# Performance work log

Measured on AMD Instinct MI355X. Metric: run time of the kernel, lower is better.

## Reference

```python
import jax, jax.numpy as jnp
import numpy as np

N, E, O, C, D_IN, OUT, L, B = 10000, 80000, 10, 64, 16, 16, 2, 16
DEG, WIDEN, BD = 3, 4, 64
EPS = 1e-6


def fibonacci_sphere(n):
    # deterministic near-uniform grid of n unit vectors on S^2 (stands in for GridGenerator's repulsion grid)
    i = jnp.arange(n, dtype=jnp.float32) + 0.5
    phi = jnp.arccos(1.0 - 2.0 * i / n)
    theta = jnp.pi * (1.0 + 5.0 ** 0.5) * i
    return jnp.stack([jnp.cos(theta) * jnp.sin(phi), jnp.sin(theta) * jnp.sin(phi), jnp.cos(phi)], axis=-1)


def poly_features(x, degree):
    # PolynomialFeatures: concat x, x(x)x, x(x)x(x)x, ... flattened outer products
    feats = [x]
    cur = x
    for _ in range(degree):
        cur = (cur[..., :, None] * x[..., None, :]).reshape(x.shape[:-1] + (-1,))
        feats.append(cur)
    return jnp.concatenate(feats, axis=-1)


def layer_norm(x, scale, bias):
    mu = jnp.mean(x, axis=-1, keepdims=True)
    var = jnp.mean((x - mu) ** 2, axis=-1, keepdims=True)
    return (x - mu) * jax.lax.rsqrt(var + EPS) * scale + bias


def setup_inputs():
    key = jax.random.key(0)
    ks = jax.random.split(key, 16)
    def w(k, shape):
        return jax.random.normal(k, shape, dtype=jnp.float32) / np.sqrt(shape[-2])
    P_SP = 2 + 4 + 8 + 16  # poly features of 2-dim spatial invariants, degree 3
    P_OR = 4               # poly features of 1-dim orientation invariant, degree 3
    return {
        "x": jax.random.normal(ks[0], (N, D_IN), jnp.float32),
        "pos": jax.random.normal(ks[1], (N, 3), jnp.float32),
        "basis_w1": w(ks[2], (P_SP, C)), "basis_b1": jnp.zeros((C,), jnp.float32),
        "basis_w2": w(ks[3], (C, BD)), "basis_b2": jnp.zeros((BD,), jnp.float32),
        "fbasis_w1": w(ks[4], (P_OR, C)), "fbasis_b1": jnp.zeros((C,), jnp.float32),
        "fbasis_w2": w(ks[5], (C, BD)), "fbasis_b2": jnp.zeros((BD,), jnp.float32),
        "embed_w": w(ks[6], (D_IN, C)),
        "conv_kw": w(ks[7], (L, BD, C)),
        "conv_fw": w(ks[8], (L, BD, C)),
        "conv_b": jnp.zeros((L, C), jnp.float32),
        "norm_s": jnp.ones((L, C), jnp.float32),
        "norm_b": jnp.zeros((L, C), jnp.float32),
        "lin1_w": w(ks[9], (L, C, WIDEN * C)), "lin1_b": jnp.zeros((L, WIDEN * C), jnp.float32),
        "lin2_w": w(ks[10], (L, WIDEN * C, C)), "lin2_b": jnp.zeros((L, C), jnp.float32),
        "ro_w": w(ks[11], (L, C, OUT)), "ro_b": jnp.zeros((L, OUT), jnp.float32),
        "edge_index": jax.random.randint(ks[12], (2, E), 0, N, jnp.int32),
        "batch": jnp.sort(jax.random.randint(ks[13], (N,), 0, B, jnp.int32)),
    }


def reference(x, pos, basis_w1, basis_b1, basis_w2, basis_b2, fbasis_w1, fbasis_b1, fbasis_w2, fbasis_b2, embed_w, conv_kw, conv_fw, conv_b, norm_s, norm_b, lin1_w, lin1_b, lin2_w, lin2_b, ro_w, ro_b, edge_index, batch):
    ori = fibonacci_sphere(O)                                             # [O,3]
    send, recv = edge_index[0], edge_index[1]
    rel = (pos[send] - pos[recv])[:, None, :]                              # [E,1,3]
    inv1 = jnp.sum(rel * ori[None], axis=-1, keepdims=True)                # [E,O,1]
    inv2 = jnp.linalg.norm(rel - inv1 * ori[None], axis=-1, keepdims=True) # [E,O,1]
    inv3 = jnp.sum(ori[None, :, :] * ori[:, None, :], axis=-1, keepdims=True)  # [O,O,1]
    sp = jnp.concatenate([inv1, inv2], axis=-1)                            # [E,O,2]
    kb = jax.nn.gelu(poly_features(sp, DEG) @ basis_w1 + basis_b1)
    kb = jax.nn.gelu(kb @ basis_w2 + basis_b2)                             # [E,O,BD]
    fkb = jax.nn.gelu(poly_features(inv3, DEG) @ fbasis_w1 + fbasis_b1)
    fkb = jax.nn.gelu(fkb @ fbasis_w2 + fbasis_b2)                         # [O,O,BD]
    h = jnp.broadcast_to((x @ embed_w)[:, None, :], (N, O, C))             # [N,O,C]
    readout = jnp.zeros((N, O, OUT), h.dtype)
    for l in range(L):
        # depthwise spatial conv: gather-send, modulate by kernel, scatter-add to receivers
        msg = h[send] * (kb @ conv_kw[l])                                  # [E,O,C]
        h1 = jax.ops.segment_sum(msg, recv, num_segments=N)                # [N,O,C]
        # depthwise fiber (orientation) conv
        fk = fkb @ conv_fw[l]                                              # [O,O,C]
        h2 = jnp.einsum('noc,poc->npc', h1, fk) / O + conv_b[l]
        # ConvNeXt MLP + residual
        y = layer_norm(h2, norm_s[l], norm_b[l])
        y = jax.nn.gelu(y @ lin1_w[l] + lin1_b[l]) @ lin2_w[l] + lin2_b[l]
        h = h + y
        readout = readout + (h @ ro_w[l] + ro_b[l])
    readout = readout / L
    out_scalar = jnp.mean(readout, axis=-2)                                # [N,OUT]
    pooled = jnp.zeros((B, OUT), out_scalar.dtype).at[batch].add(out_scalar)
    return pooled
```

## Files before the change

### kernel.cpp

```cpp
#include <hip/hip_runtime.h>
#include <math.h>

#define N_   10000
#define E_   80000
#define O_   10
#define B_   16
#define OUT_ 16
#define NROW_ (N_*O_)
#define NITEM_ (E_*O_)

typedef __attribute__((ext_vector_type(8))) short bf16x8;
typedef __attribute__((ext_vector_type(4))) short bf16x4;
typedef __attribute__((ext_vector_type(4))) float f32x4;

#define MFMA16(a,b,c) __builtin_amdgcn_mfma_f32_16x16x32_bf16(a,b,c,0,0,0)

__device__ __forceinline__ float gelu_f(float x) {
    float u = fmaf(0.044715f, x * x, 1.0f);
    float e = __builtin_amdgcn_exp2f(2.3022083f * x * u);
    float r = __builtin_amdgcn_rcpf(e + 1.0f);
    return fmaf(-x, r, x);
}

__device__ __forceinline__ unsigned short f2bf(float f) {
    union { float f; unsigned int u; } v; v.f = f;
    unsigned int r = v.u + 0x7FFFu + ((v.u >> 16) & 1u);
    return (unsigned short)(r >> 16);
}
__device__ __forceinline__ float bf2f(unsigned short u) {
    union { unsigned int u; float f; } v; v.u = ((unsigned int)u) << 16;
    return v.f;
}
__device__ __forceinline__ unsigned int cvtpk(float lo, float hi) {
    unsigned int r;
    asm("v_cvt_pk_bf16_f32 %0, %1, %2" : "=v"(r) : "v"(lo), "v"(hi));
    return r;
}
__device__ __forceinline__ bf16x4 pack4(float a, float b, float c, float d) {
    union { unsigned int u[2]; bf16x4 v; } z;
    z.u[0] = cvtpk(a, b);
    z.u[1] = cvtpk(c, d);
    return z.v;
}

__device__ __forceinline__ void fib_vec(int idx, float& vx, float& vy, float& vz) {
    float i = (float)idx + 0.5f;
    float phi = acosf(1.0f - 2.0f * i / (float)O_);
    float theta = 3.14159265358979323846f * (1.0f + 2.2360679774997896964f) * i;
    float sp = sinf(phi);
    vx = cosf(theta) * sp; vy = sinf(theta) * sp; vz = cosf(phi);
}

__global__ __launch_bounds__(256) void k_pack(
    const float* __restrict__ bw1, const float* __restrict__ bw2,
    const float* __restrict__ ckw, const float* __restrict__ l1w,
    const float* __restrict__ l2w, const float* __restrict__ row_w,
    float* __restrict__ orig,
    unsigned short* __restrict__ wW1P, unsigned short* __restrict__ wW2P,
    unsigned short* __restrict__ wCKP, unsigned short* __restrict__ wL1P,
    unsigned short* __restrict__ wL2P, unsigned short* __restrict__ wROP)
{
    const int g = blockIdx.x * 256 + threadIdx.x;
    if (g < 2048) {
        int idx = g;
        int t = idx >> 9, rem = idx & 511;
        int ln = rem >> 3, j = rem & 7;
        int row = t*16 + (ln & 15);
        int k = (ln >> 4)*8 + j;
        float s = 0.0f;
        if (k < 14) {
            const int moff[14] = {0,1,2,3,5,6,7,10,13,14,15,19,25,29};
            const int mcnt[14] = {1,1,1,2,1,1,3,3,1,1,4,6,4,1};
            const int mlist[30] = {0,1,2,3,4,5,6,7,8,10,9,11,12,13,14,
                                   15,16,18,22,17,19,20,23,24,26,21,25,27,28,29};
            for (int q = 0; q < mcnt[k]; ++q) s += bw1[mlist[moff[k]+q]*64 + row];
        }
        wW1P[idx] = f2bf(s);
    } else if (g < 6144) {
        int idx = g - 2048;
        int t = idx >> 9, rem = idx & 511;
        int mt = t >> 1, ks = t & 1;
        int ln = rem >> 3, j = rem & 7;
        int row = mt*16 + (ln & 15);
        int k = ks*32 + (ln >> 4)*8 + j;
        wW2P[idx] = f2bf(bw2[k*64 + row]);
    } else if (g < 14336) {
        int idx = g - 6144;
        int l = idx >> 12, r2 = idx & 4095;
        int t = r2 >> 9, rem = r2 & 511;
        int mt = t >> 1, ks = t & 1;
        int ln = rem >> 3, j = rem & 7;
        int row = mt*16 + (ln & 15);
        int k = ks*32 + (ln >> 4)*8 + j;
        wCKP[idx] = f2bf(ckw[l*4096 + k*64 + row]);
    } else if (g < 47104) {
        int idx = g - 14336;
        int l = idx >> 14, r2 = idx & 16383;
        int t = r2 >> 9, rem = r2 & 511;
        int mt = t >> 1, ks = t & 1;
        int ln = rem >> 3, j = rem & 7;
        int row = mt*16 + (ln & 15);
        int k = ks*32 + (ln >> 4)*8 + j;
        wL1P[idx] = f2bf(l1w[l*16384 + k*256 + row]);
    } else if (g < 79872) {
        int idx = g - 47104;
        int l = idx >> 14, r2 = idx & 16383;
        int t = r2 >> 9, rem = r2 & 511;
        int mt2 = t >> 3, ksg = t & 7;
        int ln = rem >> 3, j = rem & 7;
        int row = mt2*16 + (ln & 15);
        int k = ksg*32 + (ln >> 4)*8 + j;
        wL2P[idx] = f2bf(l2w[l*16384 + k*64 + row]);
    } else if (g < 81920) {
        int idx = g - 79872;
        int l = idx >> 10, r2 = idx & 1023;
        int ks = r2 >> 9, rem = r2 & 511;
        int ln = rem >> 3, j = rem & 7;
        int row = ln & 15;
        int k = ks*32 + (ln >> 4)*8 + j;
        wROP[idx] = f2bf(row_w[l*1024 + k*16 + row]);
    } else if (g < 81920 + O_) {
        int o = g - 81920;
        float vx, vy, vz;
        fib_vec(o, vx, vy, vz);
        orig[o*3+0] = vx; orig[o*3+1] = vy; orig[o*3+2] = vz;
    }
}

__global__ __launch_bounds__(256) void k_fibpre(
    const float* __restrict__ fw1, const float* __restrict__ fb1,
    const float* __restrict__ fw2, const float* __restrict__ fb2,
    const float* __restrict__ cfw, float* __restrict__ fkg)
{
    __shared__ float sRow[4][64];
    const int wv = threadIdx.x >> 6, lane = threadIdx.x & 63;
    const int pr = blockIdx.x * 4 + wv;
    if (pr >= 100) return;
    const int i = pr / O_, j = pr % O_;
    float ix, iy, iz, jx, jy, jz;
    fib_vec(i, ix, iy, iz);
    fib_vec(j, jx, jy, jz);
    float a = ix*jx + iy*jy + iz*jz;
    float a2 = a*a, a3 = a2*a, a4 = a3*a;
    float v = fb1[lane];
    v = fmaf(a,  fw1[0*64+lane], v);
    v = fmaf(a2, fw1[1*64+lane], v);
    v = fmaf(a3, fw1[2*64+lane], v);
    v = fmaf(a4, fw1[3*64+lane], v);
    sRow[wv][lane] = gelu_f(v);
    float acc = fb2[lane];
    for (int b = 0; b < 64; ++b) acc = fmaf(sRow[wv][b], fw2[b*64+lane], acc);
    sRow[wv][lane] = gelu_f(acc);
    for (int l = 0; l < 2; ++l) {
        float s = 0.0f;
        for (int b = 0; b < 64; ++b) s = fmaf(sRow[wv][b], cfw[l*4096 + b*64 + lane], s);
        fkg[l*6400 + pr*64 + lane] = s;
    }
}

__global__ __launch_bounds__(256) void k_embed(
    const float* __restrict__ x, const float* __restrict__ ew,
    float* __restrict__ hg, unsigned short* __restrict__ hbf0)
{
    int t = blockIdx.x * 256 + threadIdx.x;
    if (t >= N_ * 64) return;
    int n = t >> 6, c = t & 63;
    float v = 0.0f;
#pragma unroll
    for (int k = 0; k < 16; ++k) v = fmaf(x[n*16+k], ew[k*64+c], v);
    int base = n * 640 + c;
#pragma unroll
    for (int o = 0; o < O_; ++o) hg[base + o*64] = v;
    hbf0[t] = f2bf(v);
}

__global__ __launch_bounds__(256) void k_hist(const int* __restrict__ ei, int* __restrict__ counts)
{
    int e = blockIdx.x * 256 + threadIdx.x;
    if (e < E_) atomicAdd(&counts[ei[E_ + e]], 1);
}

__global__ __launch_bounds__(1024) void k_scan(
    const int* __restrict__ counts, int* __restrict__ offs, int* __restrict__ cursor)
{
    __shared__ int part[1024];
    int t = threadIdx.x;
    const int CH = 10;
    int base_i = t * CH;
    int s = 0;
#pragma unroll
    for (int i = 0; i < CH; ++i) { int idx = base_i + i; if (idx < N_) s += counts[idx]; }
    part[t] = s;
    __syncthreads();
    for (int off = 1; off < 1024; off <<= 1) {
        int v = (t >= off) ? part[t - off] : 0;
        __syncthreads();
        part[t] += v;
        __syncthreads();
    }
    int run = (t > 0) ? part[t - 1] : 0;
#pragma unroll
    for (int i = 0; i < CH; ++i) {
        int idx = base_i + i;
        if (idx < N_) { offs[idx] = run; cursor[idx] = run; run += counts[idx]; }
    }
    if (t == 1023) offs[N_] = run;
}

__global__ __launch_bounds__(256) void k_scatter(
    const int* __restrict__ ei, const float* __restrict__ pos,
    int* __restrict__ cursor, int* __restrict__ csend, int* __restrict__ crecv,
    float* __restrict__ crel)
{
    int e = blockIdx.x * 256 + threadIdx.x;
    if (e >= E_) return;
    int s = ei[e], r = ei[E_ + e];
    int slot = atomicAdd(&cursor[r], 1);
    csend[slot] = s;
    crecv[slot] = r;
    crel[slot*3+0] = pos[s*3+0] - pos[r*3+0];
    crel[slot*3+1] = pos[s*3+1] - pos[r*3+1];
    crel[slot*3+2] = pos[s*3+2] - pos[r*3+2];
}

template<int KS>
__device__ __forceinline__ void loadB(
    const unsigned short* sData, int lane, bf16x8 Bf[4][KS])
{
    const int lm = lane & 15, lk = lane >> 4;
#pragma unroll
    for (int nt = 0; nt < 4; ++nt)
#pragma unroll
        for (int ks = 0; ks < KS; ++ks) {
            int r = nt*16 + lm;
            int kb = ks*64 + lk*16;
            Bf[nt][ks] = *(const bf16x8*)((const char*)sData + r*128 + (kb ^ ((r&7)<<4)));
        }
}

template<int KS, bool BIAS, bool GELU>
__device__ __forceinline__ void stageC(
    unsigned short* sData, const bf16x8 Bf[4][KS],
    const unsigned short* __restrict__ Wp, const float* __restrict__ bias, int lane)
{
    const int lm = lane & 15, lk = lane >> 4;
#pragma unroll
    for (int mt = 0; mt < 4; ++mt) {
        bf16x8 Af[KS];
#pragma unroll
        for (int ks = 0; ks < KS; ++ks)
            Af[ks] = *(const bf16x8*)(Wp + ((mt*KS + ks)*64 + lane)*8);
        f32x4 b4 = {0,0,0,0};
        if (BIAS) b4 = *(const f32x4*)(bias + mt*16 + (lk<<2));
#pragma unroll
        for (int nt = 0; nt < 4; ++nt) {
            f32x4 acc = b4;
#pragma unroll
            for (int ks = 0; ks < KS; ++ks) acc = MFMA16(Af[ks], Bf[nt][ks], acc);
            float v0 = acc[0], v1 = acc[1], v2 = acc[2], v3 = acc[3];
            if (GELU) { v0 = gelu_f(v0); v1 = gelu_f(v1); v2 = gelu_f(v2); v3 = gelu_f(v3); }
            bf16x4 pk = pack4(v0, v1, v2, v3);
            int rr = nt*16 + lm;
            int cb = mt*32 + (lk<<3);
            *(bf16x4*)((char*)sData + rr*128 + (cb ^ ((rr&7)<<4))) = pk;
        }
    }
}

__device__ __forceinline__ void phase0(
    unsigned short* sData, int slot, int oo, const float* __restrict__ crel,
    const float* __restrict__ ori, int tid)
{
    float r0 = crel[slot*3+0], r1 = crel[slot*3+1], r2 = crel[slot*3+2];
    float o0 = ori[oo*3+0], o1 = ori[oo*3+1], o2 = ori[oo*3+2];
    float a = r0*o0 + r1*o1 + r2*o2;
    float p0 = fmaf(-a, o0, r0), p1 = fmaf(-a, o1, r1), p2 = fmaf(-a, o2, r2);
    float b = sqrtf(p0*p0 + p1*p1 + p2*p2);
    float a2 = a*a, b2 = b*b, ab = a*b;
    float m[14];
    m[0]=a; m[1]=b; m[2]=a2; m[3]=ab; m[4]=b2;
    m[5]=a2*a; m[6]=a2*b; m[7]=a*b2; m[8]=b2*b;
    m[9]=a2*a2; m[10]=a2*ab; m[11]=a2*b2; m[12]=ab*b2; m[13]=b2*b2;
    unsigned int pk[16];
#pragma unroll
    for (int j = 0; j < 7; ++j) pk[j] = cvtpk(m[2*j], m[2*j+1]);
#pragma unroll
    for (int j = 7; j < 16; ++j) pk[j] = 0;
#pragma unroll
    for (int q = 0; q < 4; ++q) {
        int cb = q*16;
        *(f32x4*)((char*)sData + tid*128 + (cb ^ ((tid&7)<<4))) = ((const f32x4*)pk)[q];
    }
}

#define SCATTER_BODY(KC_EXPR)                                                        \
    int prevr = __shfl_up(rcv, 1);                                                   \
    unsigned long long bmask = __ballot(lane > 0 && rcv != prevr);                   \
    float a0=0,a1c=0,a2c=0,a3c=0,a4c=0,a5c=0,a6c=0,a7c=0,a8c=0,a9c=0;                \
    int cur = __builtin_amdgcn_readfirstlane(rcv);                                   \
    int soi = item0 % 10;                                                            \
    _Pragma("unroll")                                                                \
    for (int ch = 0; ch < 4; ++ch) {                                                 \
        unsigned short hvu[16]; float kcv[16];                                       \
        _Pragma("unroll")                                                            \
        for (int j = 0; j < 16; ++j) {                                               \
            const int i = ch*16 + j;                                                 \
            hvu[j] = hb[__builtin_amdgcn_readlane(myaddr, i)];                       \
            kcv[j] = (KC_EXPR);                                                      \
        }                                                                            \
        _Pragma("unroll")                                                            \
        for (int j = 0; j < 16; ++j) {                                               \
            const int i = ch*16 + j;                                                 \
            if (bmask & (1ull << i)) { FLUSH_RUN(cur); cur = __builtin_amdgcn_readlane(rcv, i); } \
            float mv = kcv[j] * bf2f(hvu[j]);                                        \
            if      (soi == 0) a0  += mv;                                            \
            else if (soi == 1) a1c += mv;                                            \
            else if (soi == 2) a2c += mv;                                            \
            else if (soi == 3) a3c += mv;                                            \
            else if (soi == 4) a4c += mv;                                            \
            else if (soi == 5) a5c += mv;                                            \
            else if (soi == 6) a6c += mv;                                            \
            else if (soi == 7) a7c += mv;                                            \
            else if (soi == 8) a8c += mv;                                            \
            else               a9c += mv;                                            \
            soi = (soi == 9) ? 0 : soi + 1;                                          \
        }                                                                            \
    }                                                                                \
    FLUSH_RUN(cur);

#define FLUSH_RUN(R) { float* bp = h1g + (R)*640 + lane; \
    atomicAdd(bp+0,a0); atomicAdd(bp+64,a1c); atomicAdd(bp+128,a2c); atomicAdd(bp+192,a3c); \
    atomicAdd(bp+256,a4c); atomicAdd(bp+320,a5c); atomicAdd(bp+384,a6c); atomicAdd(bp+448,a7c); \
    atomicAdd(bp+512,a8c); atomicAdd(bp+576,a9c); \
    a0=a1c=a2c=a3c=a4c=a5c=a6c=a7c=a8c=a9c=0.0f; }

template<bool L0>
__global__ __launch_bounds__(64) void k_msg(
    const unsigned short* __restrict__ hbf, float* __restrict__ h1g,
    const int* __restrict__ csend, const int* __restrict__ crecv,
    const float* __restrict__ crel, const float* __restrict__ ori,
    const unsigned short* __restrict__ wW1P, const unsigned short* __restrict__ wW2P,
    const unsigned short* __restrict__ wCKP_l,
    const float* __restrict__ bb1, const float* __restrict__ bb2)
{
    __shared__ unsigned short sData[64*64];
    const int lane = threadIdx.x;
    const int item0 = blockIdx.x * 64;
    const int item = item0 + lane;
    const int slot = item / 10;
    const int oo = item - slot * 10;
    const int snd = csend[slot];
    const int rcv = crecv[slot];
    phase0(sData, slot, oo, crel, ori, lane);
    {
        bf16x8 Bf1[4][1]; loadB<1>(sData, lane, Bf1);
        stageC<1, true, true>(sData, Bf1, wW1P, bb1, lane);
    }
    {
        bf16x8 Bf2[4][2]; loadB<2>(sData, lane, Bf2);
        stageC<2, true, true>(sData, Bf2, wW2P, bb2, lane);
    }
    {
        bf16x8 Bf3[4][2]; loadB<2>(sData, lane, Bf3);
        stageC<2, false, false>(sData, Bf3, wCKP_l, (const float*)0, lane);
    }
    const int myaddr = L0 ? (snd * 64) : ((snd * 10 + oo) * 64);
    const unsigned short* hb = hbf + lane;
    SCATTER_BODY(bf2f(*(const unsigned short*)((const char*)sData + i*128 + ((lane*2) ^ ((i&7)<<4)))))
}

__global__ __launch_bounds__(64) void k_msg0dual(
    const unsigned short* __restrict__ hbf, float* __restrict__ h1g,
    unsigned short* __restrict__ kc1g,
    const int* __restrict__ csend, const int* __restrict__ crecv,
    const float* __restrict__ crel, const float* __restrict__ ori,
    const unsigned short* __restrict__ wW1P, const unsigned short* __restrict__ wW2P,
    const unsigned short* __restrict__ wCK0, const unsigned short* __restrict__ wCK1,
    const float* __restrict__ bb1, const float* __restrict__ bb2)
{
    __shared__ unsigned short sData[64*64];
    const int lane = threadIdx.x;
    const int item0 = blockIdx.x * 64;
    const int item = item0 + lane;
    const int slot = item / 10;
    const int oo = item - slot * 10;
    const int snd = csend[slot];
    const int rcv = crecv[slot];
    phase0(sData, slot, oo, crel, ori, lane);
    {
        bf16x8 Bf1[4][1]; loadB<1>(sData, lane, Bf1);
        stageC<1, true, true>(sData, Bf1, wW1P, bb1, lane);
    }
    {
        bf16x8 Bf2[4][2]; loadB<2>(sData, lane, Bf2);
        stageC<2, true, true>(sData, Bf2, wW2P, bb2, lane);
    }
    bf16x8 Bf3[4][2]; loadB<2>(sData, lane, Bf3);
    stageC<2, false, false>(sData, Bf3, wCK1, (const float*)0, lane);
#pragma unroll
    for (int q = 0; q < 8; ++q) {
        f32x4 v = *(const f32x4*)((const char*)sData + lane*128 + ((q*16) ^ ((lane&7)<<4)));
        *(f32x4*)((char*)kc1g + (size_t)item*128 + ((q*16) ^ ((lane&7)<<4))) = v;
    }
    stageC<2, false, false>(sData, Bf3, wCK0, (const float*)0, lane);
    const int myaddr = snd * 64;
    const unsigned short* hb = hbf + lane;
    SCATTER_BODY(bf2f(*(const unsigned short*)((const char*)sData + i*128 + ((lane*2) ^ ((i&7)<<4)))))
}

__global__ __launch_bounds__(64) void k_msg1lite(
    const unsigned short* __restrict__ kc1g, const unsigned short* __restrict__ hbf,
    float* __restrict__ h1g,
    const int* __restrict__ csend, const int* __restrict__ crecv)
{
    const int lane = threadIdx.x;
    const int item0 = blockIdx.x * 64;
    const int item = item0 + lane;
    const int slot = item / 10;
    const int oo = item - slot * 10;
    const int snd = csend[slot];
    const int rcv = crecv[slot];
    const int myaddr = (snd * 10 + oo) * 64;
    const unsigned short* hb = hbf + lane;
    const char* kb = (const char*)kc1g + (size_t)item0 * 128;
    SCATTER_BODY(bf2f(*(const unsigned short*)(kb + (size_t)i*128 + ((lane*2) ^ ((i&7)<<4)))))
}
#undef FLUSH_RUN
#undef SCATTER_BODY

__global__ __launch_bounds__(256) void k_fln(
    float* __restrict__ h1, const float* __restrict__ fkg,
    const float* __restrict__ cb, const float* __restrict__ ns,
    const float* __restrict__ nb, unsigned short* __restrict__ y, int zero_h1)
{
    __shared__ float sFK[6400];
    const int tid = threadIdx.x;
    for (int i = tid; i < 6400; i += 256) sFK[i] = fkg[i];
    __syncthreads();
    const int lane = tid & 63, wv = tid >> 6;
    float cbv = cb[lane], nsv = ns[lane], nbv = nb[lane];
    for (int g4 = blockIdx.x; g4 < N_/4; g4 += gridDim.x) {
        const int n = g4 * 4 + wv;
        float hr[10];
#pragma unroll
        for (int o = 0; o < O_; ++o) hr[o] = h1[n*640 + o*64 + lane];
        if (zero_h1) {
#pragma unroll
            for (int o = 0; o < O_; ++o) h1[n*640 + o*64 + lane] = 0.0f;
        }
#pragma unroll
        for (int p = 0; p < O_; ++p) {
            float v = 0.0f;
#pragma unroll
            for (int o = 0; o < O_; ++o) v = fmaf(hr[o], sFK[(p*O_+o)*64 + lane], v);
            v = v * 0.1f + cbv;
            float s = v, q = v*v;
#pragma unroll
            for (int d = 1; d < 64; d <<= 1) { s += __shfl_xor(s, d); q += __shfl_xor(q, d); }
            float mu = s * (1.0f/64.0f);
            float var = q * (1.0f/64.0f) - mu*mu;
            float rs = rsqrtf(var + 1e-6f);
            float yv = (v - mu) * rs * nsv + nbv;
            y[(n*O_ + p)*64 + lane] = f2bf(yv);
        }
    }
}

__global__ __launch_bounds__(256, 4) void k_mlp(
    unsigned short* ybuf, float* __restrict__ hg, float* __restrict__ rout,
    const unsigned short* __restrict__ wL1P_l, const float* __restrict__ l1b_l,
    const unsigned short* __restrict__ wL2P_l, const float* __restrict__ l2b_l,
    const unsigned short* __restrict__ wROP_l, const float* __restrict__ rob_l)
{
    __shared__ unsigned short sA[64*64];
    const int tid = threadIdx.x;
    const int lane = tid & 63, wv = tid >> 6;
    const int rb = blockIdx.x * 64;
#pragma unroll
    for (int i = tid*16; i < 64*128; i += 256*16) {
        int r = i >> 7, off = i & 127;
        int grow = rb + r; if (grow >= NROW_) grow = NROW_ - 1;
        *(f32x4*)((char*)sA + r*128 + (off ^ ((r&7)<<4))) =
            *(const f32x4*)((const char*)ybuf + (size_t)grow*128 + off);
    }
    __syncthreads();
    const int lm = lane & 15, lk = lane >> 4;
    const int r0 = wv*16 + lm;
    bf16x8 Yf[2];
#pragma unroll
    for (int ks = 0; ks < 2; ++ks) {
        int kb = ks*64 + lk*16;
        Yf[ks] = *(const bf16x8*)((const char*)sA + r0*128 + (kb ^ ((r0&7)<<4)));
    }
    f32x4 acc2[4];
#pragma unroll
    for (int m = 0; m < 4; ++m) acc2[m] = *(const f32x4*)(l2b_l + m*16 + (lk<<2));
#pragma unroll
    for (int jb = 0; jb < 4; ++jb) {
#pragma unroll
        for (int mt = 0; mt < 4; ++mt) {
            bf16x8 A1[2];
#pragma unroll
            for (int ks = 0; ks < 2; ++ks)
                A1[ks] = *(const bf16x8*)(wL1P_l + (((jb*4 + mt)*2 + ks)*64 + lane)*8);
            f32x4 acc = *(const f32x4*)(l1b_l + jb*64 + mt*16 + (lk<<2));
            acc = MFMA16(A1[0], Yf[0], acc);
            acc = MFMA16(A1[1], Yf[1], acc);
            bf16x4 pk = pack4(gelu_f(acc[0]), gelu_f(acc[1]), gelu_f(acc[2]), gelu_f(acc[3]));
            int cb = mt*32 + (lk<<3);
            *(bf16x4*)((char*)sA + r0*128 + (cb ^ ((r0&7)<<4))) = pk;
        }
        bf16x8 Mf[2];
#pragma unroll
        for (int ks = 0; ks < 2; ++ks) {
            int kb = ks*64 + lk*16;
            Mf[ks] = *(const bf16x8*)((const char*)sA + r0*128 + (kb ^ ((r0&7)<<4)));
        }
#pragma unroll
        for (int mt2 = 0; mt2 < 4; ++mt2) {
            bf16x8 A2[2];
#pragma unroll
            for (int ks = 0; ks < 2; ++ks)
                A2[ks] = *(const bf16x8*)(wL2P_l + ((mt2*8 + jb*2 + ks)*64 + lane)*8);
            acc2[mt2] = MFMA16(A2[0], Mf[0], acc2[mt2]);
            acc2[mt2] = MFMA16(A2[1], Mf[1], acc2[mt2]);
        }
    }
    const int grow = rb + r0;
    const bool valid = grow < NROW_;
    const int growc = valid ? grow : (NROW_ - 1);
#pragma unroll
    for (int mt2 = 0; mt2 < 4; ++mt2) {
        f32x4 hv = *(const f32x4*)(hg + (size_t)growc*64 + mt2*16 + (lk<<2));
        f32x4 hn;
#pragma unroll
        for (int r = 0; r < 4; ++r) hn[r] = hv[r] + acc2[mt2][r];
        bf16x4 pk = pack4(hn[0], hn[1], hn[2], hn[3]);
        if (valid) {
            *(f32x4*)(hg + (size_t)grow*64 + mt2*16 + (lk<<2)) = hn;
            *(bf16x4*)((char*)ybuf + (size_t)grow*128 + (mt2*16 + (lk<<2))*2) = pk;
        }
        int cb = mt2*32 + (lk<<3);
        *(bf16x4*)((char*)sA + r0*128 + (cb ^ ((r0&7)<<4))) = pk;
    }
    bf16x8 Ro[2];
#pragma unroll
    for (int ks = 0; ks < 2; ++ks)
        Ro[ks] = *(const bf16x8*)(wROP_l + (ks*64 + lane)*8);
    f32x4 r4 = *(const f32x4*)(rob_l + (lk<<2));
    bf16x8 Hf[2];
#pragma unroll
    for (int ks = 0; ks < 2; ++ks) {
        int kb = ks*64 + lk*16;
        Hf[ks] = *(const bf16x8*)((const char*)sA + r0*128 + (kb ^ ((r0&7)<<4)));
    }
    r4 = MFMA16(Ro[0], Hf[0], r4);
    r4 = MFMA16(Ro[1], Hf[1], r4);
    if (valid) *(f32x4*)(rout + (size_t)grow*16 + (lk<<2)) = r4;
}

__global__ __launch_bounds__(256) void k_pool(
    const float* __restrict__ r0, const float* __restrict__ r1,
    const int* __restrict__ batch, float* __restrict__ out)
{
    int t = blockIdx.x * 256 + threadIdx.x;
    if (t >= N_ * 16) return;
    int n = t >> 4, j = t & 15;
    float s = 0.0f;
#pragma unroll
    for (int p = 0; p < O_; ++p)
        s += r0[(n*O_ + p)*16 + j] + r1[(n*O_ + p)*16 + j];
    atomicAdd(&out[batch[n]*16 + j], s * (1.0f/20.0f));
}

extern "C" void kernel_launch(void* const* d_in, const int* in_sizes, int n_in,
                              void* d_out, int out_size, void* d_ws, size_t ws_size,
                              hipStream_t stream)
{
    const float* x    = (const float*)d_in[0];
    const float* pos  = (const float*)d_in[1];
    const float* bw1  = (const float*)d_in[2];
    const float* bb1  = (const float*)d_in[3];
    const float* bw2  = (const float*)d_in[4];
    const float* bb2  = (const float*)d_in[5];
    const float* fw1  = (const float*)d_in[6];
    const float* fb1  = (const float*)d_in[7];
    const float* fw2  = (const float*)d_in[8];
    const float* fb2  = (const float*)d_in[9];
    const float* embw = (const float*)d_in[10];
    const float* ckw  = (const float*)d_in[11];
    const float* cfw  = (const float*)d_in[12];
    const float* cb   = (const float*)d_in[13];
    const float* ns   = (const float*)d_in[14];
    const float* nbp  = (const float*)d_in[15];
    const float* l1w  = (const float*)d_in[16];
    const float* l1b  = (const float*)d_in[17];
    const float* l2w  = (const float*)d_in[18];
    const float* l2b  = (const float*)d_in[19];
    const float* row  = (const float*)d_in[20];
    const float* rob  = (const float*)d_in[21];
    const int*   ei   = (const int*)d_in[22];
    const int*   batch= (const int*)d_in[23];
    float* out = (float*)d_out;

    char* w = (char*)d_ws;
    size_t off = 0;
    auto alloc = [&](size_t bytes) -> char* {
        char* p = w + off; off += (bytes + 255) / 256 * 256; return p;
    };
    float* ori    = (float*)alloc(32 * 4);
    float* fkg    = (float*)alloc(2 * 6400 * 4);
    unsigned short* wW1P = (unsigned short*)alloc(4*512*2);
    unsigned short* wW2P = (unsigned short*)alloc(8*512*2);
    unsigned short* wCKP = (unsigned short*)alloc(2*8*512*2);
    unsigned short* wL1P = (unsigned short*)alloc(2*32*512*2);
    unsigned short* wL2P = (unsigned short*)alloc(2*32*512*2);
    unsigned short* wROP = (unsigned short*)alloc(2*2*512*2);
    float* h      = (float*)alloc((size_t)N_ * 640 * 4);
    float* h1     = (float*)alloc((size_t)N_ * 640 * 4);
    unsigned short* y = (unsigned short*)alloc((size_t)NROW_ * 64 * 2);
    unsigned short* hbf0 = (unsigned short*)alloc((size_t)N_ * 64 * 2);
    float* rout0  = (float*)alloc((size_t)NROW_ * 16 * 4);
    float* rout1  = (float*)alloc((size_t)NROW_ * 16 * 4);
    float* crel   = (float*)alloc((size_t)E_ * 3 * 4);
    int*   counts = (int*)alloc((N_ + 1) * 4);
    int*   offs   = (int*)alloc((N_ + 1) * 4);
    int*   cursor = (int*)alloc((N_ + 1) * 4);
    int*   csend  = (int*)alloc((size_t)E_ * 4);
    int*   crecv  = (int*)alloc((size_t)E_ * 4);
    unsigned short* kc1g = nullptr;
    if (ws_size >= off + (size_t)NITEM_ * 64 * 2 + 256)
        kc1g = (unsigned short*)alloc((size_t)NITEM_ * 64 * 2);

    hipMemsetAsync(h1, 0, (size_t)N_ * 640 * 4, stream);
    hipMemsetAsync(out, 0, (size_t)out_size * 4, stream);
    hipMemsetAsync(counts, 0, (N_ + 1) * 4, stream);

    k_pack<<<321, 256, 0, stream>>>(bw1, bw2, ckw, l1w, l2w, row, ori,
                                    wW1P, wW2P, wCKP, wL1P, wL2P, wROP);
    k_fibpre<<<25, 256, 0, stream>>>(fw1, fb1, fw2, fb2, cfw, fkg);
    k_embed<<<(N_ * 64 + 255) / 256, 256, 0, stream>>>(x, embw, h, hbf0);
    k_hist<<<(E_ + 255) / 256, 256, 0, stream>>>(ei, counts);
    k_scan<<<1, 1024, 0, stream>>>(counts, offs, cursor);
    k_scatter<<<(E_ + 255) / 256, 256, 0, stream>>>(ei, pos, cursor, csend, crecv, crel);

    for (int l = 0; l < 2; ++l) {
        if (l == 0) {
            if (kc1g)
                k_msg0dual<<<NITEM_ / 64, 64, 0, stream>>>(hbf0, h1, kc1g, csend, crecv,
                                                           crel, ori, wW1P, wW2P,
                                                           wCKP, wCKP + 4096, bb1, bb2);
            else
                k_msg<true><<<NITEM_ / 64, 64, 0, stream>>>(hbf0, h1, csend, crecv, crel, ori,
                                                            wW1P, wW2P, wCKP, bb1, bb2);
        } else {
            if (kc1g)
                k_msg1lite<<<NITEM_ / 64, 64, 0, stream>>>(kc1g, y, h1, csend, crecv);
            else
                k_msg<false><<<NITEM_ / 64, 64, 0, stream>>>(y, h1, csend, crecv, crel, ori,
                                                             wW1P, wW2P, wCKP + 4096, bb1, bb2);
        }
        k_fln<<<625, 256, 0, stream>>>(h1, fkg + l*6400, cb + l*64, ns + l*64, nbp + l*64, y,
                                       (l == 0) ? 1 : 0);
        k_mlp<<<(NROW_ + 63) / 64, 256, 0, stream>>>(y, h, (l == 0 ? rout0 : rout1),
                                                     wL1P + l*16384, l1b + l*256,
                                                     wL2P + l*16384, l2b + l*64,
                                                     wROP + l*1024, rob + l*16);
    }
    k_pool<<<(N_ * 16 + 255) / 256, 256, 0, stream>>>(rout0, rout1, batch, out);
}
```

Measured before the change: 414.9 us.

## Double MLP row tile per block and coalesce kernel-coefficient stores

The MLP kernel now handles 128 rows per block, 32 per wave, so each weight fragment loaded from global memory feeds two MFMA row tiles. This halves weight reloads per row, at the cost of more registers and LDS and a lower occupancy bound. Separately, the cached layer-1 kernel coefficients are now written contiguously (linear lane-strided) rather than per-item swizzled rows. The consumer read drops the XOR swizzle to match, which coalesces the global store.

```diff
diff --git a/kernel.cpp b/kernel.cpp
--- a/kernel.cpp
+++ b/kernel.cpp
@@ -397,10 +397,16 @@
     }
     bf16x8 Bf3[4][2]; loadB<2>(sData, lane, Bf3);
     stageC<2, false, false>(sData, Bf3, wCK1, (const float*)0, lane);
-#pragma unroll
-    for (int q = 0; q < 8; ++q) {
-        f32x4 v = *(const f32x4*)((const char*)sData + lane*128 + ((q*16) ^ ((lane&7)<<4)));
-        *(f32x4*)((char*)kc1g + (size_t)item*128 + ((q*16) ^ ((lane&7)<<4))) = v;
+    {
+        char* dst = (char*)kc1g + (size_t)item0 * 128;
+#pragma unroll
+        for (int q = 0; q < 8; ++q) {
+            int g = q*1024 + lane*16;
+            int row = g >> 7;
+            int off = g & 127;
+            f32x4 v = *(const f32x4*)((const char*)sData + row*128 + (off ^ ((row&7)<<4)));
+            *(f32x4*)(dst + g) = v;
+        }
     }
     stageC<2, false, false>(sData, Bf3, wCK0, (const float*)0, lane);
     const int myaddr = snd * 64;
@@ -423,7 +429,7 @@
     const int myaddr = (snd * 10 + oo) * 64;
     const unsigned short* hb = hbf + lane;
     const char* kb = (const char*)kc1g + (size_t)item0 * 128;
-    SCATTER_BODY(bf2f(*(const unsigned short*)(kb + (size_t)i*128 + ((lane*2) ^ ((i&7)<<4)))))
+    SCATTER_BODY(bf2f(*(const unsigned short*)(kb + (size_t)i*128 + lane*2)))
 }
 #undef FLUSH_RUN
 #undef SCATTER_BODY
@@ -466,18 +472,18 @@
     }
 }
 
-__global__ __launch_bounds__(256, 4) void k_mlp(
+__global__ __launch_bounds__(256, 3) void k_mlp(
     unsigned short* ybuf, float* __restrict__ hg, float* __restrict__ rout,
     const unsigned short* __restrict__ wL1P_l, const float* __restrict__ l1b_l,
     const unsigned short* __restrict__ wL2P_l, const float* __restrict__ l2b_l,
     const unsigned short* __restrict__ wROP_l, const float* __restrict__ rob_l)
 {
-    __shared__ unsigned short sA[64*64];
+    __shared__ unsigned short sA[128*64];
     const int tid = threadIdx.x;
     const int lane = tid & 63, wv = tid >> 6;
-    const int rb = blockIdx.x * 64;
-#pragma unroll
-    for (int i = tid*16; i < 64*128; i += 256*16) {
+    const int rb = blockIdx.x * 128;
+#pragma unroll
+    for (int i = tid*16; i < 128*128; i += 256*16) {
         int r = i >> 7, off = i & 127;
         int grow = rb + r; if (grow >= NROW_) grow = NROW_ - 1;
         *(f32x4*)((char*)sA + r*128 + (off ^ ((r&7)<<4))) =
@@ -485,16 +491,22 @@
     }
     __syncthreads();
     const int lm = lane & 15, lk = lane >> 4;
-    const int r0 = wv*16 + lm;
-    bf16x8 Yf[2];
-#pragma unroll
-    for (int ks = 0; ks < 2; ++ks) {
-        int kb = ks*64 + lk*16;
-        Yf[ks] = *(const bf16x8*)((const char*)sA + r0*128 + (kb ^ ((r0&7)<<4)));
-    }
-    f32x4 acc2[4];
-#pragma unroll
-    for (int m = 0; m < 4; ++m) acc2[m] = *(const f32x4*)(l2b_l + m*16 + (lk<<2));
+    bf16x8 Yf[2][2];
+#pragma unroll
+    for (int nt = 0; nt < 2; ++nt)
+#pragma unroll
+        for (int ks = 0; ks < 2; ++ks) {
+            int r = wv*32 + nt*16 + lm;
+            int kb = ks*64 + lk*16;
+            Yf[nt][ks] = *(const bf16x8*)((const char*)sA + r*128 + (kb ^ ((r&7)<<4)));
+        }
+    f32x4 acc2[4][2];
+#pragma unroll
+    for (int m = 0; m < 4; ++m) {
+        f32x4 b2 = *(const f32x4*)(l2b_l + m*16 + (lk<<2));
+#pragma unroll
+        for (int nt = 0; nt < 2; ++nt) acc2[m][nt] = b2;
+    }
 #pragma unroll
     for (int jb = 0; jb < 4; ++jb) {
 #pragma unroll
@@ -503,60 +515,81 @@
 #pragma unroll
             for (int ks = 0; ks < 2; ++ks)
                 A1[ks] = *(const bf16x8*)(wL1P_l + (((jb*4 + mt)*2 + ks)*64 + lane)*8);
-            f32x4 acc = *(const f32x4*)(l1b_l + jb*64 + mt*16 + (lk<<2));
-            acc = MFMA16(A1[0], Yf[0], acc);
-            acc = MFMA16(A1[1], Yf[1], acc);
-            bf16x4 pk = pack4(gelu_f(acc[0]), gelu_f(acc[1]), gelu_f(acc[2]), gelu_f(acc[3]));
-            int cb = mt*32 + (lk<<3);
-            *(bf16x4*)((char*)sA + r0*128 + (cb ^ ((r0&7)<<4))) = pk;
-        }
-        bf16x8 Mf[2];
+            f32x4 b4 = *(const f32x4*)(l1b_l + jb*64 + mt*16 + (lk<<2));
+#pragma unroll
+            for (int nt = 0; nt < 2; ++nt) {
+                f32x4 acc = b4;
+                acc = MFMA16(A1[0], Yf[nt][0], acc);
+                acc = MFMA16(A1[1], Yf[nt][1], acc);
+                bf16x4 pk = pack4(gelu_f(acc[0]), gelu_f(acc[1]), gelu_f(acc[2]), gelu_f(acc[3]));
+                int rr = wv*32 + nt*16 + lm;
+                int cb = mt*32 + (lk<<3);
+                *(bf16x4*)((char*)sA + rr*128 + (cb ^ ((rr&7)<<4))) = pk;
+            }
+        }
+        bf16x8 Mf[2][2];
+#pragma unroll
+        for (int nt = 0; nt < 2; ++nt)
+#pragma unroll
+            for (int ks = 0; ks < 2; ++ks) {
+                int r = wv*32 + nt*16 + lm;
+                int kb = ks*64 + lk*16;
+                Mf[nt][ks] = *(const bf16x8*)((const char*)sA + r*128 + (kb ^ ((r&7)<<4)));
+            }
+#pragma unroll
+        for (int mt2 = 0; mt2 < 4; ++mt2) {
+            bf16x8 A2[2];
+#pragma unroll
+            for (int ks = 0; ks < 2; ++ks)
+                A2[ks] = *(const bf16x8*)(wL2P_l + ((mt2*8 + jb*2 + ks)*64 + lane)*8);
+#pragma unroll
+            for (int nt = 0; nt < 2; ++nt) {
+                acc2[mt2][nt] = MFMA16(A2[0], Mf[nt][0], acc2[mt2][nt]);
+                acc2[mt2][nt] = MFMA16(A2[1], Mf[nt][1], acc2[mt2][nt]);
+            }
+        }
+    }
+#pragma unroll
+    for (int nt = 0; nt < 2; ++nt) {
+        const int rloc = wv*32 + nt*16 + lm;
+        const int grow = rb + rloc;
+        const bool valid = grow < NROW_;
+        const int growc = valid ? grow : (NROW_ - 1);
+#pragma unroll
+        for (int mt2 = 0; mt2 < 4; ++mt2) {
+            f32x4 hv = *(const f32x4*)(hg + (size_t)growc*64 + mt2*16 + (lk<<2));
+            f32x4 hn;
+#pragma unroll
+            for (int r = 0; r < 4; ++r) hn[r] = hv[r] + acc2[mt2][nt][r];
+            bf16x4 pk = pack4(hn[0], hn[1], hn[2], hn[3]);
+            if (valid) {
+                *(f32x4*)(hg + (size_t)grow*64 + mt2*16 + (lk<<2)) = hn;
+                *(bf16x4*)((char*)ybuf + (size_t)grow*128 + (mt2*16 + (lk<<2))*2) = pk;
+            }
+            int cb = mt2*32 + (lk<<3);
+            *(bf16x4*)((char*)sA + rloc*128 + (cb ^ ((rloc&7)<<4))) = pk;
+        }
+    }
+    bf16x8 Ro[2];
+#pragma unroll
+    for (int ks = 0; ks < 2; ++ks)
+        Ro[ks] = *(const bf16x8*)(wROP_l + (ks*64 + lane)*8);
+    f32x4 rb4 = *(const f32x4*)(rob_l + (lk<<2));
+#pragma unroll
+    for (int nt = 0; nt < 2; ++nt) {
+        const int rloc = wv*32 + nt*16 + lm;
+        const int grow = rb + rloc;
+        bf16x8 Hf[2];
 #pragma unroll
         for (int ks = 0; ks < 2; ++ks) {
             int kb = ks*64 + lk*16;
-            Mf[ks] = *(const bf16x8*)((const char*)sA + r0*128 + (kb ^ ((r0&7)<<4)));
-        }
-#pragma unroll
-        for (int mt2 = 0; mt2 < 4; ++mt2) {
-            bf16x8 A2[2];
-#pragma unroll
-            for (int ks = 0; ks < 2; ++ks)
-                A2[ks] = *(const bf16x8*)(wL2P_l + ((mt2*8 + jb*2 + ks)*64 + lane)*8);
-            acc2[mt2] = MFMA16(A2[0], Mf[0], acc2[mt2]);
-            acc2[mt2] = MFMA16(A2[1], Mf[1], acc2[mt2]);
-        }
-    }
-    const int grow = rb + r0;
-    const bool valid = grow < NROW_;
-    const int growc = valid ? grow : (NROW_ - 1);
-#pragma unroll
-    for (int mt2 = 0; mt2 < 4; ++mt2) {
-        f32x4 hv = *(const f32x4*)(hg + (size_t)growc*64 + mt2*16 + (lk<<2));
-        f32x4 hn;
-#pragma unroll
-        for (int r = 0; r < 4; ++r) hn[r] = hv[r] + acc2[mt2][r];
-        bf16x4 pk = pack4(hn[0], hn[1], hn[2], hn[3]);
-        if (valid) {
-            *(f32x4*)(hg + (size_t)grow*64 + mt2*16 + (lk<<2)) = hn;
-            *(bf16x4*)((char*)ybuf + (size_t)grow*128 + (mt2*16 + (lk<<2))*2) = pk;
-        }
-        int cb = mt2*32 + (lk<<3);
-        *(bf16x4*)((char*)sA + r0*128 + (cb ^ ((r0&7)<<4))) = pk;
-    }
-    bf16x8 Ro[2];
-#pragma unroll
-    for (int ks = 0; ks < 2; ++ks)
-        Ro[ks] = *(const bf16x8*)(wROP_l + (ks*64 + lane)*8);
-    f32x4 r4 = *(const f32x4*)(rob_l + (lk<<2));
-    bf16x8 Hf[2];
-#pragma unroll
-    for (int ks = 0; ks < 2; ++ks) {
-        int kb = ks*64 + lk*16;
-        Hf[ks] = *(const bf16x8*)((const char*)sA + r0*128 + (kb ^ ((r0&7)<<4)));
-    }
-    r4 = MFMA16(Ro[0], Hf[0], r4);
-    r4 = MFMA16(Ro[1], Hf[1], r4);
-    if (valid) *(f32x4*)(rout + (size_t)grow*16 + (lk<<2)) = r4;
+            Hf[ks] = *(const bf16x8*)((const char*)sA + rloc*128 + (kb ^ ((rloc&7)<<4)));
+        }
+        f32x4 r4 = rb4;
+        r4 = MFMA16(Ro[0], Hf[0], r4);
+        r4 = MFMA16(Ro[1], Hf[1], r4);
+        if (grow < NROW_) *(f32x4*)(rout + (size_t)grow*16 + (lk<<2)) = r4;
+    }
 }
 
 __global__ __launch_bounds__(256) void k_pool(
@@ -662,10 +695,10 @@
         }
         k_fln<<<625, 256, 0, stream>>>(h1, fkg + l*6400, cb + l*64, ns + l*64, nbp + l*64, y,
                                        (l == 0) ? 1 : 0);
-        k_mlp<<<(NROW_ + 63) / 64, 256, 0, stream>>>(y, h, (l == 0 ? rout0 : rout1),
-                                                     wL1P + l*16384, l1b + l*256,
-                                                     wL2P + l*16384, l2b + l*64,
-                                                     wROP + l*1024, rob + l*16);
+        k_mlp<<<(NROW_ + 127) / 128, 256, 0, stream>>>(y, h, (l == 0 ? rout0 : rout1),
+                                                       wL1P + l*16384, l1b + l*256,
+                                                       wL2P + l*16384, l2b + l*64,
+                                                       wROP + l*1024, rob + l*16);
     }
     k_pool<<<(N_ * 16 + 255) / 256, 256, 0, stream>>>(rout0, rout1, batch, out);
 }
```

After: 406.1 us. 1.02x faster.
